# Performance work log

Measured on AMD Instinct MI355X. Metric: run time of the kernel, lower is better.

## Reference

```python
import jax, jax.numpy as jnp
import numpy as np

HID, OUT, D = 256, 64, 128
N_ITEM, N_USER, E = 100000, 50000, 800000


def sage_conv(x_src, x_dst, src, dst, w_l, b_l, w_r, n_dst):
    # PyG SAGEConv (mean aggr): out = lin_l(mean_j x_src[j]) + lin_r(x_dst)
    msg = x_src[src]                                        # [E, d_src] gather
    agg = jax.ops.segment_sum(msg, dst, num_segments=n_dst)  # [n_dst, d_src]
    cnt = jax.ops.segment_sum(jnp.ones((src.shape[0],), x_src.dtype), dst,
                              num_segments=n_dst)
    mean = agg / jnp.clip(cnt, 1.0, None)[:, None]
    return mean @ w_l + b_l + x_dst @ w_r


def setup_inputs() -> dict:
    key = jax.random.key(0)
    ks = jax.random.split(key, 16)
    sc = lambda d: 1.0 / np.sqrt(d)
    inp = {
        "x_item": jax.random.normal(ks[0], (N_ITEM, D), jnp.float32),
        "x_user": jax.random.normal(ks[1], (N_USER, D), jnp.float32),
        "ei_ii_src": jax.random.randint(ks[2], (E,), 0, N_ITEM),
        "ei_ii_dst": jax.random.randint(ks[3], (E,), 0, N_ITEM),
        "ei_iu_src": jax.random.randint(ks[4], (E,), 0, N_ITEM),
        "ei_iu_dst": jax.random.randint(ks[5], (E,), 0, N_USER),
        # conv1: item->item, in (D, D) -> HID
        "w_l1": jax.random.normal(ks[6], (D, HID), jnp.float32) * sc(D),
        "b1": jnp.zeros((HID,), jnp.float32),
        "w_r1": jax.random.normal(ks[7], (D, HID), jnp.float32) * sc(D),
        # conv2: (item D, user D) -> HID
        "w_l2": jax.random.normal(ks[8], (D, HID), jnp.float32) * sc(D),
        "b2": jnp.zeros((HID,), jnp.float32),
        "w_r2": jax.random.normal(ks[9], (D, HID), jnp.float32) * sc(D),
        # conv3: (item HID, user HID) -> HID
        "w_l3": jax.random.normal(ks[10], (HID, HID), jnp.float32) * sc(HID),
        "b3": jnp.zeros((HID,), jnp.float32),
        "w_r3": jax.random.normal(ks[11], (HID, HID), jnp.float32) * sc(HID),
        # final linear HID -> OUT
        "w_lin": jax.random.normal(ks[12], (HID, OUT), jnp.float32) * sc(HID),
        "b_lin": jnp.zeros((OUT,), jnp.float32),
    }
    return inp


def reference(x_item, x_user, ei_ii_src, ei_ii_dst, ei_iu_src, ei_iu_dst,
              w_l1, b1, w_r1, w_l2, b2, w_r2, w_l3, b3, w_r3, w_lin, b_lin):
    item_x = jax.nn.relu(sage_conv(x_item, x_item, ei_ii_src, ei_ii_dst,
                                   w_l1, b1, w_r1, N_ITEM))
    user_x = jax.nn.relu(sage_conv(x_item, x_user, ei_iu_src, ei_iu_dst,
                                   w_l2, b2, w_r2, N_USER))
    user_x = jax.nn.relu(sage_conv(item_x, user_x, ei_iu_src, ei_iu_dst,
                                   w_l3, b3, w_r3, N_USER))
    return user_x @ w_lin + b_lin
```

## Files before the change

### kernel.cpp

```cpp
#include <hip/hip_runtime.h>
#include <hip/hip_bf16.h>

#define N_ITEM 100000
#define N_USER 50000
#define D_IN   128
#define HID    256
#define OUT_D  64
#define CAP    64
#define CPAD   16

#define SCB   256
#define CVIB  2048
#define CVUB  1024
#define PKB   136
#define PREP_GRID (SCB + CVIB + CVUB + PKB)

#define C2B   391
#define A3B   3125

typedef __attribute__((ext_vector_type(8))) short bf16x8;
typedef __attribute__((ext_vector_type(4))) float f32x4;

__device__ inline float b2f(unsigned int h) {
    union { unsigned int u; float f; } c; c.u = h << 16; return c.f;
}
__device__ inline unsigned short f2b(float f) {
    unsigned int u = __builtin_bit_cast(unsigned int, f);
    u += 0x7fff + ((u >> 16) & 1);
    return (unsigned short)(u >> 16);
}

__device__ inline void pack_unit(const float* __restrict__ wl,
                                 const float* __restrict__ wr,
                                 int K, int NCv, unsigned short* __restrict__ dst,
                                 int u)
{
    int kb = u / NCv, col = u - kb * NCv;
    int colp = col ^ (kb & 7);
    unsigned short tmp[8];
    #pragma unroll
    for (int j = 0; j < 8; ++j) {
        int k = kb * 8 + j;
        float w = (k < K) ? wl[(size_t)k * NCv + col]
                          : wr[(size_t)(k - K) * NCv + col];
        tmp[j] = f2b(w);
    }
    *(uint4*)&dst[((size_t)kb * NCv + colp) * 8] = *(const uint4*)tmp;
}

__global__ __launch_bounds__(256) void prep_kernel(
    const int* __restrict__ ii_src, const int* __restrict__ ii_dst,
    const int* __restrict__ iu_src, const int* __restrict__ iu_dst,
    int* __restrict__ cur_i, int* __restrict__ cur_u,
    int* __restrict__ slot_ii, int* __restrict__ slot_iu, int E,
    const float* __restrict__ x_item, const float* __restrict__ x_user,
    unsigned short* __restrict__ Acat1, unsigned short* __restrict__ Acat2,
    const float* __restrict__ wl1, const float* __restrict__ wr1,
    const float* __restrict__ wl2, const float* __restrict__ wr2,
    const float* __restrict__ wl3, const float* __restrict__ wr3,
    const float* __restrict__ wlin,
    unsigned short* __restrict__ Wp1, unsigned short* __restrict__ Wp2,
    unsigned short* __restrict__ Wp3, unsigned short* __restrict__ Wpl)
{
    int b = blockIdx.x;
    if (b < SCB) {
        const int NT = SCB * 256;
        int e = b * 256 + threadIdx.x;
        for (; e + 3 * NT < E; e += 4 * NT) {
            int d[8], s[8], p[8];
            #pragma unroll
            for (int u = 0; u < 4; ++u) {
                d[u]     = ii_dst[e + u * NT]; s[u]     = ii_src[e + u * NT];
                d[u + 4] = iu_dst[e + u * NT]; s[u + 4] = iu_src[e + u * NT];
            }
            #pragma unroll
            for (int u = 0; u < 4; ++u) p[u] = atomicAdd(&cur_i[d[u] * CPAD], 1);
            #pragma unroll
            for (int u = 4; u < 8; ++u) p[u] = atomicAdd(&cur_u[d[u] * CPAD], 1);
            #pragma unroll
            for (int u = 0; u < 4; ++u)
                if (p[u] < CAP)
                    __builtin_nontemporal_store(s[u], &slot_ii[d[u] * CAP + p[u]]);
            #pragma unroll
            for (int u = 4; u < 8; ++u)
                if (p[u] < CAP)
                    __builtin_nontemporal_store(s[u], &slot_iu[d[u] * CAP + p[u]]);
        }
        for (; e < E; e += NT) {
            int d0 = ii_dst[e], s0 = ii_src[e];
            int p0 = atomicAdd(&cur_i[d0 * CPAD], 1);
            if (p0 < CAP) __builtin_nontemporal_store(s0, &slot_ii[d0 * CAP + p0]);
            int d1 = iu_dst[e], s1 = iu_src[e];
            int p1 = atomicAdd(&cur_u[d1 * CPAD], 1);
            if (p1 < CAP) __builtin_nontemporal_store(s1, &slot_iu[d1 * CAP + p1]);
        }
    } else if (b < SCB + CVIB) {
        const int STR = CVIB * 256;
        for (int u = (b - SCB) * 256 + threadIdx.x; u < N_ITEM * 32; u += STR) {
            int row = u >> 5, c4 = (u & 31) * 4;
            float4 v = *(const float4*)&x_item[(size_t)row * 128 + c4];
            ushort4 o;
            o.x = f2b(v.x); o.y = f2b(v.y); o.z = f2b(v.z); o.w = f2b(v.w);
            *(ushort4*)&Acat1[(size_t)row * 256 + 128 + c4] = o;
        }
    } else if (b < SCB + CVIB + CVUB) {
        const int STR = CVUB * 256;
        for (int u = (b - SCB - CVIB) * 256 + threadIdx.x; u < N_USER * 32; u += STR) {
            int row = u >> 5, c4 = (u & 31) * 4;
            float4 v = *(const float4*)&x_user[(size_t)row * 128 + c4];
            ushort4 o;
            o.x = f2b(v.x); o.y = f2b(v.y); o.z = f2b(v.z); o.w = f2b(v.w);
            *(ushort4*)&Acat2[(size_t)row * 256 + 128 + c4] = o;
        }
    } else {
        int t = (b - SCB - CVIB - CVUB) * 256 + threadIdx.x;
        if (t < 8192)       pack_unit(wl1, wr1, 128, 256, Wp1, t);
        else if (t < 16384) pack_unit(wl2, wr2, 128, 256, Wp2, t - 8192);
        else if (t < 32768) pack_unit(wl3, wr3, 256, 256, Wp3, t - 16384);
        else if (t < 34816) pack_unit(wlin, wlin, 256, 64, Wpl, t - 32768);
    }
}

__global__ __launch_bounds__(256) void agg12_kernel(
    const unsigned short* __restrict__ xsrc,
    const int* __restrict__ slot_ii, const int* __restrict__ cur_i,
    const int* __restrict__ slot_iu, const int* __restrict__ cur_u,
    unsigned short* __restrict__ Acat1, unsigned short* __restrict__ Acat2)
{
    int b = blockIdx.x;
    int sub = threadIdx.x >> 5;
    const int* sl; int num; unsigned short* dst;
    if (b < 12500) {
        int row = b * 8 + sub;
        sl  = slot_ii + (size_t)row * CAP;
        num = min(cur_i[(size_t)row * CPAD], CAP);
        dst = Acat1 + (size_t)row * 256;
    } else {
        int row = (b - 12500) * 8 + sub;
        sl  = slot_iu + (size_t)row * CAP;
        num = min(cur_u[(size_t)row * CPAD], CAP);
        dst = Acat2 + (size_t)row * 256;
    }
    int hl = threadIdx.x & 31;
    const unsigned short* xb = xsrc + hl * 4;
    float acc[4] = {};

    int j = 0;
    for (; j + 8 <= num; j += 8) {
        int s[8];
        #pragma unroll
        for (int u = 0; u < 8; ++u) s[u] = sl[j + u];
        uint2 v[8];
        #pragma unroll
        for (int u = 0; u < 8; ++u)
            v[u] = *(const uint2*)(xb + (size_t)s[u] * 256);
        #pragma unroll
        for (int u = 0; u < 8; ++u) {
            acc[0] += b2f(v[u].x & 0xffffu);
            acc[1] += b2f(v[u].x >> 16);
            acc[2] += b2f(v[u].y & 0xffffu);
            acc[3] += b2f(v[u].y >> 16);
        }
    }
    for (; j < num; ++j) {
        uint2 v = *(const uint2*)(xb + (size_t)sl[j] * 256);
        acc[0] += b2f(v.x & 0xffffu);
        acc[1] += b2f(v.x >> 16);
        acc[2] += b2f(v.y & 0xffffu);
        acc[3] += b2f(v.y >> 16);
    }

    float sc = 1.0f / fmaxf((float)num, 1.0f);
    uint2 w;
    w.x = (unsigned int)f2b(acc[0] * sc) | ((unsigned int)f2b(acc[1] * sc) << 16);
    w.y = (unsigned int)f2b(acc[2] * sc) | ((unsigned int)f2b(acc[3] * sc) << 16);
    *(uint2*)(dst + hl * 4) = w;
}

template <int NC, int WM, int WN, bool OUT_BF16, bool RELU>
__device__ __forceinline__ void gemm_body(
    int bid,
    const unsigned short* __restrict__ A, int lda,
    const unsigned short* __restrict__ Wp,
    const float* __restrict__ bias,
    void* __restrict__ Cout, int ldc, int col_off,
    int nrows, int nkt)
{
    constexpr int BM = 128;
    constexpr int MR = WM / 16, NR = WN / 16;
    constexpr int NWC = NC / WN;
    __shared__ unsigned short As[BM * 64];
    __shared__ unsigned short Bs[64 * NC];

    const int tid  = threadIdx.x;
    const int wave = tid >> 6;
    const int lane = tid & 63;
    const int row0 = bid * BM;
    const int wr = wave / NWC;
    const int wc = wave % NWC;

    f32x4 acc[MR][NR];
    #pragma unroll
    for (int m = 0; m < MR; ++m)
        #pragma unroll
        for (int n = 0; n < NR; ++n)
            acc[m][n] = (f32x4){0.f, 0.f, 0.f, 0.f};

    for (int kt = 0; kt < nkt; ++kt) {
        #pragma unroll
        for (int c = 0; c < 2; ++c) {
            int i = wave * 2 + c;
            int rl = 8 * i + (lane >> 3);
            int kc = (lane & 7) ^ (lane >> 3);
            const unsigned short* g =
                A + (size_t)(row0 + rl) * lda + kt * 64 + kc * 8;
            __builtin_amdgcn_global_load_lds(
                (const __attribute__((address_space(1))) void*)g,
                (__attribute__((address_space(3))) void*)(As + i * 512), 16, 0, 0);
        }
        constexpr int BCALLS = (64 * NC * 2) / 1024;
        constexpr int PW = BCALLS / 8;
        #pragma unroll
        for (int c = 0; c < PW; ++c) {
            int j = wave * PW + c;
            const unsigned short* g =
                Wp + (size_t)kt * (8 * NC * 8) + (size_t)j * 512 + lane * 8;
            __builtin_amdgcn_global_load_lds(
                (const __attribute__((address_space(1))) void*)g,
                (__attribute__((address_space(3))) void*)(Bs + j * 512), 16, 0, 0);
        }
        __syncthreads();

        #pragma unroll
        for (int kk = 0; kk < 2; ++kk) {
            bf16x8 af[MR], bfr[NR];
            #pragma unroll
            for (int m = 0; m < MR; ++m) {
                int row = wr * WM + m * 16 + (lane & 15);
                int kc = ((kk * 4) + (lane >> 4)) ^ (lane & 7);
                af[m] = *(const bf16x8*)(As + row * 64 + kc * 8);
            }
            #pragma unroll
            for (int n = 0; n < NR; ++n) {
                int kb = kk * 4 + (lane >> 4);
                int col = (wc * WN + n * 16 + (lane & 15)) ^ (kb & 7);
                bfr[n] = *(const bf16x8*)(Bs + (kb * NC + col) * 8);
            }
            #pragma unroll
            for (int m = 0; m < MR; ++m)
                #pragma unroll
                for (int n = 0; n < NR; ++n)
                    acc[m][n] = __builtin_amdgcn_mfma_f32_16x16x32_bf16(
                        af[m], bfr[n], acc[m][n], 0, 0, 0);
        }
        __syncthreads();
    }

    #pragma unroll
    for (int n = 0; n < NR; ++n) {
        int col = wc * WN + n * 16 + (lane & 15);
        float bv = bias[col];
        #pragma unroll
        for (int m = 0; m < MR; ++m) {
            #pragma unroll
            for (int j = 0; j < 4; ++j) {
                int row = row0 + wr * WM + m * 16 + (lane >> 4) * 4 + j;
                if (row < nrows) {
                    float v = acc[m][n][j] + bv;
                    if (RELU) v = fmaxf(v, 0.f);
                    if (OUT_BF16)
                        ((unsigned short*)Cout)[(size_t)row * ldc + col_off + col] = f2b(v);
                    else
                        ((float*)Cout)[(size_t)row * ldc + col_off + col] = v;
                }
            }
        }
    }
}

template <int NC, int WM, int WN, bool OUT_BF16, bool RELU>
__global__ __launch_bounds__(512) void gemm_mfma(
    const unsigned short* __restrict__ A, int lda,
    const unsigned short* __restrict__ Wp,
    const float* __restrict__ bias,
    void* __restrict__ Cout, int ldc, int col_off,
    int nrows, int nkt)
{
    gemm_body<NC, WM, WN, OUT_BF16, RELU>(blockIdx.x, A, lda, Wp, bias,
                                          Cout, ldc, col_off, nrows, nkt);
}

__global__ __launch_bounds__(512) void conv2_agg3_kernel(
    const unsigned short* __restrict__ Acat2,
    const unsigned short* __restrict__ Wp2,
    const float* __restrict__ b2,
    unsigned short* __restrict__ Acat3,
    const unsigned short* __restrict__ item_x,
    const int* __restrict__ slot_iu, const int* __restrict__ cur_u)
{
    if (blockIdx.x < C2B) {
        gemm_body<256, 64, 64, true, true>(blockIdx.x, Acat2, 256, Wp2, b2,
                                           Acat3, 512, 256, N_USER, 4);
        return;
    }
    int b = blockIdx.x - C2B;
    int row = b * 16 + (threadIdx.x >> 5);
    int hl = threadIdx.x & 31;
    const int* sl = slot_iu + (size_t)row * CAP;
    int num = min(cur_u[(size_t)row * CPAD], CAP);
    const unsigned short* xb = item_x + hl * 8;
    float acc[8] = {};

    int j = 0;
    for (; j + 8 <= num; j += 8) {
        int s[8];
        #pragma unroll
        for (int u = 0; u < 8; ++u) s[u] = sl[j + u];
        uint4 v[8];
        #pragma unroll
        for (int u = 0; u < 8; ++u)
            v[u] = *(const uint4*)(xb + (size_t)s[u] * 256);
        #pragma unroll
        for (int u = 0; u < 8; ++u) {
            acc[0] += b2f(v[u].x & 0xffffu);
            acc[1] += b2f(v[u].x >> 16);
            acc[2] += b2f(v[u].y & 0xffffu);
            acc[3] += b2f(v[u].y >> 16);
            acc[4] += b2f(v[u].z & 0xffffu);
            acc[5] += b2f(v[u].z >> 16);
            acc[6] += b2f(v[u].w & 0xffffu);
            acc[7] += b2f(v[u].w >> 16);
        }
    }
    for (; j < num; ++j) {
        uint4 v = *(const uint4*)(xb + (size_t)sl[j] * 256);
        acc[0] += b2f(v.x & 0xffffu);
        acc[1] += b2f(v.x >> 16);
        acc[2] += b2f(v.y & 0xffffu);
        acc[3] += b2f(v.y >> 16);
        acc[4] += b2f(v.z & 0xffffu);
        acc[5] += b2f(v.z >> 16);
        acc[6] += b2f(v.w & 0xffffu);
        acc[7] += b2f(v.w >> 16);
    }

    float sc = 1.0f / fmaxf((float)num, 1.0f);
    uint4 w;
    w.x = (unsigned int)f2b(acc[0] * sc) | ((unsigned int)f2b(acc[1] * sc) << 16);
    w.y = (unsigned int)f2b(acc[2] * sc) | ((unsigned int)f2b(acc[3] * sc) << 16);
    w.z = (unsigned int)f2b(acc[4] * sc) | ((unsigned int)f2b(acc[5] * sc) << 16);
    w.w = (unsigned int)f2b(acc[6] * sc) | ((unsigned int)f2b(acc[7] * sc) << 16);
    *(uint4*)(Acat3 + (size_t)row * 512 + hl * 8) = w;
}

extern "C" void kernel_launch(void* const* d_in, const int* in_sizes, int n_in,
                              void* d_out, int out_size, void* d_ws, size_t ws_size,
                              hipStream_t stream)
{
    const float* x_item = (const float*)d_in[0];
    const float* x_user = (const float*)d_in[1];
    const int* ii_src   = (const int*)d_in[2];
    const int* ii_dst   = (const int*)d_in[3];
    const int* iu_src   = (const int*)d_in[4];
    const int* iu_dst   = (const int*)d_in[5];
    const float* w_l1 = (const float*)d_in[6];
    const float* b1   = (const float*)d_in[7];
    const float* w_r1 = (const float*)d_in[8];
    const float* w_l2 = (const float*)d_in[9];
    const float* b2   = (const float*)d_in[10];
    const float* w_r2 = (const float*)d_in[11];
    const float* w_l3 = (const float*)d_in[12];
    const float* b3   = (const float*)d_in[13];
    const float* w_r3 = (const float*)d_in[14];
    const float* w_lin = (const float*)d_in[15];
    const float* b_lin = (const float*)d_in[16];
    float* out = (float*)d_out;

    const int E = in_sizes[2];
    const int NIP = 100096;
    const int NUP = 50048;

    int* cur_i   = (int*)d_ws;
    int* cur_u   = cur_i + (size_t)N_ITEM * CPAD;
    int* slot_ii = cur_u + (size_t)N_USER * CPAD;
    int* slot_iu = slot_ii + (size_t)N_ITEM * CAP;

    unsigned short* Acat1  = (unsigned short*)(slot_iu + (size_t)N_USER * CAP);
    unsigned short* item_x = Acat1  + (size_t)NIP * 256;
    unsigned short* Acat2  = item_x + (size_t)NIP * 256;
    unsigned short* Acat3  = Acat2  + (size_t)NUP * 256;
    unsigned short* ux3    = Acat3  + (size_t)NUP * 512;
    unsigned short* Wp1    = ux3    + (size_t)NUP * 256;
    unsigned short* Wp2    = Wp1 + 65536;
    unsigned short* Wp3    = Wp2 + 65536;
    unsigned short* Wpl    = Wp3 + 131072;

    hipMemsetAsync(cur_i, 0, (size_t)(N_ITEM + N_USER) * CPAD * 4, stream);

    prep_kernel<<<PREP_GRID, 256, 0, stream>>>(
        ii_src, ii_dst, iu_src, iu_dst, cur_i, cur_u, slot_ii, slot_iu, E,
        x_item, x_user, Acat1, Acat2,
        w_l1, w_r1, w_l2, w_r2, w_l3, w_r3, w_lin,
        Wp1, Wp2, Wp3, Wpl);

    agg12_kernel<<<18750, 256, 0, stream>>>(
        Acat1 + 128, slot_ii, cur_i, slot_iu, cur_u, Acat1, Acat2);

    gemm_mfma<256, 64, 64, true, true><<<NIP / 128, 512, 0, stream>>>(
        Acat1, 256, Wp1, b1, item_x, 256, 0, N_ITEM, 4);

    conv2_agg3_kernel<<<C2B + A3B, 512, 0, stream>>>(
        Acat2, Wp2, b2, Acat3, item_x, slot_iu, cur_u);

    gemm_mfma<256, 64, 64, true, true><<<NUP / 128, 512, 0, stream>>>(
        Acat3, 512, Wp3, b3, ux3, 256, 0, N_USER, 8);

    gemm_mfma<64, 16, 64, false, false><<<NUP / 128, 512, 0, stream>>>(
        ux3, 256, Wpl, b_lin, out, 64, 0, N_USER, 4);
}
```

Before: 386.3 us.

## Pack edge counters densely and vectorize edge-index loads in scatter prep

Removes the 16-int padding on the per-destination counters so they are dense ints, which shrinks the memset and the counter footprint read later by the aggregation kernels. The scatter part of prep now gives each thread four consecutive edges loaded with int4 vector loads and uses more blocks, and it drops the nontemporal stores for slot writes. The trade-off is more atomic contention per cache line on the dense counters, in exchange for less memory traffic and a smaller memset.

```diff
diff --git a/kernel.cpp b/kernel.cpp
--- a/kernel.cpp
+++ b/kernel.cpp
@@ -7,9 +7,8 @@
 #define HID    256
 #define OUT_D  64
 #define CAP    64
-#define CPAD   16
-
-#define SCB   256
+
+#define SCB   782
 #define CVIB  2048
 #define CVUB  1024
 #define PKB   136
@@ -64,35 +63,38 @@
 {
     int b = blockIdx.x;
     if (b < SCB) {
-        const int NT = SCB * 256;
-        int e = b * 256 + threadIdx.x;
-        for (; e + 3 * NT < E; e += 4 * NT) {
-            int d[8], s[8], p[8];
-            #pragma unroll
-            for (int u = 0; u < 4; ++u) {
-                d[u]     = ii_dst[e + u * NT]; s[u]     = ii_src[e + u * NT];
-                d[u + 4] = iu_dst[e + u * NT]; s[u + 4] = iu_src[e + u * NT];
+        int t = b * 256 + threadIdx.x;
+        int e4 = t * 4;
+        if (e4 + 3 < E) {
+            int4 di = *(const int4*)&ii_dst[e4];
+            int4 si = *(const int4*)&ii_src[e4];
+            int4 du = *(const int4*)&iu_dst[e4];
+            int4 su = *(const int4*)&iu_src[e4];
+            int p0 = atomicAdd(&cur_i[di.x], 1);
+            int p1 = atomicAdd(&cur_i[di.y], 1);
+            int p2 = atomicAdd(&cur_i[di.z], 1);
+            int p3 = atomicAdd(&cur_i[di.w], 1);
+            int q0 = atomicAdd(&cur_u[du.x], 1);
+            int q1 = atomicAdd(&cur_u[du.y], 1);
+            int q2 = atomicAdd(&cur_u[du.z], 1);
+            int q3 = atomicAdd(&cur_u[du.w], 1);
+            if (p0 < CAP) slot_ii[di.x * CAP + p0] = si.x;
+            if (p1 < CAP) slot_ii[di.y * CAP + p1] = si.y;
+            if (p2 < CAP) slot_ii[di.z * CAP + p2] = si.z;
+            if (p3 < CAP) slot_ii[di.w * CAP + p3] = si.w;
+            if (q0 < CAP) slot_iu[du.x * CAP + q0] = su.x;
+            if (q1 < CAP) slot_iu[du.y * CAP + q1] = su.y;
+            if (q2 < CAP) slot_iu[du.z * CAP + q2] = su.z;
+            if (q3 < CAP) slot_iu[du.w * CAP + q3] = su.w;
+        } else {
+            for (int e = e4; e < E; ++e) {
+                int d0 = ii_dst[e], s0 = ii_src[e];
+                int p = atomicAdd(&cur_i[d0], 1);
+                if (p < CAP) slot_ii[d0 * CAP + p] = s0;
+                int d1 = iu_dst[e], s1 = iu_src[e];
+                int q = atomicAdd(&cur_u[d1], 1);
+                if (q < CAP) slot_iu[d1 * CAP + q] = s1;
             }
-            #pragma unroll
-            for (int u = 0; u < 4; ++u) p[u] = atomicAdd(&cur_i[d[u] * CPAD], 1);
-            #pragma unroll
-            for (int u = 4; u < 8; ++u) p[u] = atomicAdd(&cur_u[d[u] * CPAD], 1);
-            #pragma unroll
-            for (int u = 0; u < 4; ++u)
-                if (p[u] < CAP)
-                    __builtin_nontemporal_store(s[u], &slot_ii[d[u] * CAP + p[u]]);
-            #pragma unroll
-            for (int u = 4; u < 8; ++u)
-                if (p[u] < CAP)
-                    __builtin_nontemporal_store(s[u], &slot_iu[d[u] * CAP + p[u]]);
-        }
-        for (; e < E; e += NT) {
-            int d0 = ii_dst[e], s0 = ii_src[e];
-            int p0 = atomicAdd(&cur_i[d0 * CPAD], 1);
-            if (p0 < CAP) __builtin_nontemporal_store(s0, &slot_ii[d0 * CAP + p0]);
-            int d1 = iu_dst[e], s1 = iu_src[e];
-            int p1 = atomicAdd(&cur_u[d1 * CPAD], 1);
-            if (p1 < CAP) __builtin_nontemporal_store(s1, &slot_iu[d1 * CAP + p1]);
         }
     } else if (b < SCB + CVIB) {
         const int STR = CVIB * 256;
@@ -133,12 +135,12 @@
     if (b < 12500) {
         int row = b * 8 + sub;
         sl  = slot_ii + (size_t)row * CAP;
-        num = min(cur_i[(size_t)row * CPAD], CAP);
+        num = min(cur_i[row], CAP);
         dst = Acat1 + (size_t)row * 256;
     } else {
         int row = (b - 12500) * 8 + sub;
         sl  = slot_iu + (size_t)row * CAP;
-        num = min(cur_u[(size_t)row * CPAD], CAP);
+        num = min(cur_u[row], CAP);
         dst = Acat2 + (size_t)row * 256;
     }
     int hl = threadIdx.x & 31;
@@ -307,7 +309,7 @@
     int row = b * 16 + (threadIdx.x >> 5);
     int hl = threadIdx.x & 31;
     const int* sl = slot_iu + (size_t)row * CAP;
-    int num = min(cur_u[(size_t)row * CPAD], CAP);
+    int num = min(cur_u[row], CAP);
     const unsigned short* xb = item_x + hl * 8;
     float acc[8] = {};
 
@@ -381,8 +383,8 @@
     const int NUP = 50048;
 
     int* cur_i   = (int*)d_ws;
-    int* cur_u   = cur_i + (size_t)N_ITEM * CPAD;
-    int* slot_ii = cur_u + (size_t)N_USER * CPAD;
+    int* cur_u   = cur_i + 100352;
+    int* slot_ii = cur_u + 50176;
     int* slot_iu = slot_ii + (size_t)N_ITEM * CAP;
 
     unsigned short* Acat1  = (unsigned short*)(slot_iu + (size_t)N_USER * CAP);
@@ -395,7 +397,7 @@
     unsigned short* Wp3    = Wp2 + 65536;
     unsigned short* Wpl    = Wp3 + 131072;
 
-    hipMemsetAsync(cur_i, 0, (size_t)(N_ITEM + N_USER) * CPAD * 4, stream);
+    hipMemsetAsync(cur_i, 0, (size_t)150528 * 4, stream);
 
     prep_kernel<<<PREP_GRID, 256, 0, stream>>>(
         ii_src, ii_dst, iu_src, iu_dst, cur_i, cur_u, slot_ii, slot_iu, E,
```

After: 383.0 us. No clear change (-0.9%).
